# Performance work log

Hardware: AMD Instinct MI355X
Metric: run time of the kernel (lower is better)

## Reference

```python
import jax, jax.numpy as jnp
import numpy as np

NUM_EMBEDDINGS = 1024
EMBEDDING_DIM = 128
COMMITMENT_COST = 0.25


def setup_inputs() -> dict:
    key = jax.random.key(0)
    k1, k2 = jax.random.split(key)
    z = jax.random.normal(k1, (16, EMBEDDING_DIM, 64, 64), dtype=jnp.float32)
    # codebook initialized uniform(-1/K, 1/K) as in the torch module
    codebook = jax.random.uniform(
        k2, (NUM_EMBEDDINGS, EMBEDDING_DIM), dtype=jnp.float32,
        minval=-1.0 / NUM_EMBEDDINGS, maxval=1.0 / NUM_EMBEDDINGS)
    return {"z": z, "codebook": codebook}


def reference(z, codebook):
    B, C = z.shape[0], z.shape[1]
    K = codebook.shape[0]
    # (B, C, H, W) -> (B*H*W, C)
    z_flat = z.reshape(B, C, -1).transpose(0, 2, 1).reshape(-1, C)
    N = z_flat.shape[0]

    # squared L2 distances (same argmin as cdist p=2)
    d2 = (jnp.sum(z_flat * z_flat, axis=1, keepdims=True)
          - 2.0 * (z_flat @ codebook.T)
          + jnp.sum(codebook * codebook, axis=1))  # [N, K]
    indices = jnp.argmin(d2, axis=1)               # [N]

    quantized_flat = codebook[indices]             # [N, C] gather
    q_raw = quantized_flat.reshape(B, -1, C).transpose(0, 2, 1).reshape(z.shape)

    # training-mode losses (F.mse_loss = mean squared error)
    commitment_loss = jnp.mean((z - jax.lax.stop_gradient(q_raw)) ** 2)
    codebook_loss = jnp.mean((q_raw - jax.lax.stop_gradient(z)) ** 2)
    vq_loss = codebook_loss + COMMITMENT_COST * commitment_loss

    # straight-through estimator
    quantized = z + jax.lax.stop_gradient(q_raw - z)

    # perplexity over code usage (zero-count codes contribute 0 to entropy)
    counts = jax.ops.segment_sum(jnp.ones((N,), jnp.float32), indices,
                                 num_segments=K)
    probs = counts / jnp.float32(N)
    perplexity = jnp.exp(-jnp.sum(probs * jnp.log(probs + 1e-10)))

    return quantized, indices, vq_loss, perplexity
```

## Files before the change

### kernel.cpp

```cpp
#include <hip/hip_runtime.h>
#include <math.h>

namespace {
constexpr int CDIM   = 128;
constexpr int KCODES = 1024;
constexpr int HWSZ   = 4096;
constexpr int BATCH  = 16;
constexpr int NPOS   = BATCH * HWSZ;
constexpr int P      = 256;
constexpr int NWAVES = 8;
constexpr int KPW    = KCODES / NWAVES;
constexpr int THREADS = 512;
constexpr size_t QELEMS   = (size_t)BATCH * CDIM * HWSZ;
constexpr size_t IDX_OFF  = QELEMS;
constexpr size_t LOSS_OFF = IDX_OFF + (size_t)NPOS;
constexpr size_t PERP_OFF = LOSS_OFF + 1;
constexpr int WS_C2   = 0;
constexpr int WS_HIST = 1024;
constexpr int WS_LOSS = 2048;
constexpr float INV_TOTAL = 1.0f / (float)QELEMS;
constexpr float INV_NPOS  = 1.0f / (float)NPOS;
}

__device__ __forceinline__ float np_sumsq_128(const float* v) {
    float r[8];
    #pragma unroll
    for (int j = 0; j < 8; ++j) r[j] = __fmul_rn(v[j], v[j]);
    #pragma unroll
    for (int i = 8; i < 128; i += 8) {
        #pragma unroll
        for (int j = 0; j < 8; ++j)
            r[j] = __fadd_rn(r[j], __fmul_rn(v[i + j], v[i + j]));
    }
    const float s01 = __fadd_rn(r[0], r[1]);
    const float s23 = __fadd_rn(r[2], r[3]);
    const float s45 = __fadd_rn(r[4], r[5]);
    const float s67 = __fadd_rn(r[6], r[7]);
    return __fadd_rn(__fadd_rn(s01, s23), __fadd_rn(s45, s67));
}

__global__ __launch_bounds__(256) void vq_prep(const float* __restrict__ cb,
                                               float* __restrict__ ws) {
    const int k = blockIdx.x * 256 + threadIdx.x;
    const float* row = cb + (size_t)k * CDIM;
    float rr[CDIM];
    #pragma unroll
    for (int c = 0; c < CDIM; ++c) rr[c] = row[c];
    ws[WS_C2 + k] = np_sumsq_128(rr);
    ((unsigned int*)ws)[WS_HIST + k] = 0u;
    if (k == 0) ws[WS_LOSS] = 0.0f;
}

__global__ __launch_bounds__(512, 1) void vq_main(const float* __restrict__ z,
                                                  const float* __restrict__ cb,
                                                  float* __restrict__ ws,
                                                  float* __restrict__ out) {
    __shared__ __align__(16) float zt[CDIM][P];
    __shared__ float z2s[P];
    __shared__ float bdls[NWAVES][P];
    __shared__ int   bkls[NWAVES][P];
    __shared__ int   wkls[P];
    __shared__ float red[THREADS];

    const int tid   = threadIdx.x;
    const int nbase = blockIdx.x * P;
    const int b     = nbase >> 12;
    const int hw0   = nbase & (HWSZ - 1);
    const float* zb = z + (size_t)b * CDIM * HWSZ + hw0;

    #pragma unroll
    for (int i = 0; i < (CDIM * P / 4) / THREADS; ++i) {
        const int linear = i * THREADS + tid;
        const int c  = linear >> 6;
        const int p4 = (linear & 63) * 4;
        *(float4*)&zt[c][p4] = *(const float4*)(zb + (size_t)c * HWSZ + p4);
    }
    __syncthreads();

    if (tid < P) {
        const int p = tid;
        float r[8];
        #pragma unroll
        for (int j = 0; j < 8; ++j) {
            const float x = zt[j][p];
            r[j] = __fmul_rn(x, x);
        }
        #pragma unroll
        for (int i = 8; i < CDIM; i += 8) {
            #pragma unroll
            for (int j = 0; j < 8; ++j) {
                const float x = zt[i + j][p];
                r[j] = __fadd_rn(r[j], __fmul_rn(x, x));
            }
        }
        const float s01 = __fadd_rn(r[0], r[1]);
        const float s23 = __fadd_rn(r[2], r[3]);
        const float s45 = __fadd_rn(r[4], r[5]);
        const float s67 = __fadd_rn(r[6], r[7]);
        z2s[p] = __fadd_rn(__fadd_rn(s01, s23), __fadd_rn(s45, s67));
    }
    __syncthreads();

    const int lane = tid & 63;
    const int p0   = lane * 4;
    const int wid  = __builtin_amdgcn_readfirstlane(tid >> 6);
    const int kw   = wid * KPW;
    const float* c2g = ws + WS_C2;

    float z2r[4];
    #pragma unroll
    for (int i = 0; i < 4; ++i) z2r[i] = z2s[p0 + i];

    float bestd[4] = {INFINITY, INFINITY, INFINITY, INFINITY};
    int   bestk[4] = {0, 0, 0, 0};

    for (int oct = 0; oct < KPW / 8; ++oct) {
        const int kb = kw + oct * 8;
        const float* coct = cb + (size_t)kb * CDIM;

        float a[4][8];
        #pragma unroll
        for (int i = 0; i < 4; ++i)
            #pragma unroll
            for (int j = 0; j < 8; ++j) a[i][j] = 0.0f;

        #pragma unroll 2
        for (int c4 = 0; c4 < CDIM / 4; ++c4) {
            const int c = c4 * 4;
            const float4 zv0 = *(const float4*)&zt[c + 0][p0];
            const float4 zv1 = *(const float4*)&zt[c + 1][p0];
            const float4 zv2 = *(const float4*)&zt[c + 2][p0];
            const float4 zv3 = *(const float4*)&zt[c + 3][p0];
            float4 cv[8];
            #pragma unroll
            for (int j = 0; j < 8; ++j)
                cv[j] = *(const float4*)(coct + (size_t)j * CDIM + c);
            #pragma unroll
            for (int j = 0; j < 8; ++j) {
                a[0][j] = fmaf(zv0.x, cv[j].x, a[0][j]);
                a[0][j] = fmaf(zv1.x, cv[j].y, a[0][j]);
                a[0][j] = fmaf(zv2.x, cv[j].z, a[0][j]);
                a[0][j] = fmaf(zv3.x, cv[j].w, a[0][j]);
                a[1][j] = fmaf(zv0.y, cv[j].x, a[1][j]);
                a[1][j] = fmaf(zv1.y, cv[j].y, a[1][j]);
                a[1][j] = fmaf(zv2.y, cv[j].z, a[1][j]);
                a[1][j] = fmaf(zv3.y, cv[j].w, a[1][j]);
                a[2][j] = fmaf(zv0.z, cv[j].x, a[2][j]);
                a[2][j] = fmaf(zv1.z, cv[j].y, a[2][j]);
                a[2][j] = fmaf(zv2.z, cv[j].z, a[2][j]);
                a[2][j] = fmaf(zv3.z, cv[j].w, a[2][j]);
                a[3][j] = fmaf(zv0.w, cv[j].x, a[3][j]);
                a[3][j] = fmaf(zv1.w, cv[j].y, a[3][j]);
                a[3][j] = fmaf(zv2.w, cv[j].z, a[3][j]);
                a[3][j] = fmaf(zv3.w, cv[j].w, a[3][j]);
            }
        }

        #pragma unroll
        for (int j = 0; j < 8; ++j) {
            const float c2 = c2g[kb + j];
            #pragma unroll
            for (int i = 0; i < 4; ++i) {
                const float d = __fadd_rn(fmaf(-2.0f, a[i][j], z2r[i]), c2);
                if (d < bestd[i]) { bestd[i] = d; bestk[i] = kb + j; }
            }
        }
    }

    #pragma unroll
    for (int i = 0; i < 4; ++i) {
        bdls[wid][p0 + i] = bestd[i];
        bkls[wid][p0 + i] = bestk[i];
    }
    __syncthreads();

    unsigned int* ghist = (unsigned int*)ws + WS_HIST;
    if (tid < P) {
        const int p = tid;
        float bd = bdls[0][p];
        int   bk = bkls[0][p];
        #pragma unroll
        for (int g = 1; g < NWAVES; ++g) {
            const float d = bdls[g][p];
            const int   k = bkls[g][p];
            if (d < bd || (d == bd && k < bk)) { bd = d; bk = k; }
        }
        wkls[p] = bk;
        out[IDX_OFF + (size_t)(nbase + p)] = (float)bk;
        atomicAdd(&ghist[bk], 1u);
        red[tid] = bd;
    } else {
        red[tid] = 0.0f;
    }
    __syncthreads();
    for (int s = THREADS / 2; s > 0; s >>= 1) {
        if (tid < s) red[tid] += red[tid + s];
        __syncthreads();
    }
    if (tid == 0) atomicAdd(&ws[WS_LOSS], red[0]);

    float* ob = out + (size_t)b * CDIM * HWSZ + hw0;
    #pragma unroll
    for (int i = 0; i < (CDIM * P) / THREADS; ++i) {
        const int linear = i * THREADS + tid;
        const int c = linear >> 8;
        const int p = linear & 255;
        ob[(size_t)c * HWSZ + p] = cb[(size_t)wkls[p] * CDIM + c];
    }
}

__global__ __launch_bounds__(1024) void vq_final(const float* __restrict__ ws,
                                                 float* __restrict__ out) {
    __shared__ float red[1024];
    const int t = threadIdx.x;
    const unsigned int* hist = (const unsigned int*)ws + WS_HIST;
    const float p = (float)hist[t] * INV_NPOS;
    red[t] = p * logf(p + 1e-10f);
    __syncthreads();
    for (int s = 512; s > 0; s >>= 1) {
        if (t < s) red[t] += red[t + s];
        __syncthreads();
    }
    if (t == 0) {
        out[LOSS_OFF] = 1.25f * (ws[WS_LOSS] * INV_TOTAL);
        out[PERP_OFF] = expf(-red[0]);
    }
}

extern "C" void kernel_launch(void* const* d_in, const int* in_sizes, int n_in,
                              void* d_out, int out_size, void* d_ws, size_t ws_size,
                              hipStream_t stream) {
    const float* z  = (const float*)d_in[0];
    const float* cb = (const float*)d_in[1];
    float* out = (float*)d_out;
    float* ws  = (float*)d_ws;

    vq_prep <<<KCODES / 256, 256, 0, stream>>>(cb, ws);
    vq_main <<<NPOS / P,     THREADS, 0, stream>>>(z, cb, ws, out);
    vq_final<<<1,           1024, 0, stream>>>(ws, out);
}
```

Before: 302.6 us.

## Double waves per block to split codebook across sixteen waves

Raises the main kernel from 512 to 1024 threads per block, so sixteen waves each scan 64 codes instead of eight waves scanning 128. This aims to add latency hiding for the global codebook loads and FMA chains per CU. To fit the larger per-wave argmin staging into shared memory, the best-index arrays become 16-bit and the loss reduction buffer shrinks to P entries. Launch bounds of 1024 halve the register budget per thread, which may cause spills given the 32 accumulators plus the float4 codebook registers.

```diff
diff --git a/kernel.cpp b/kernel.cpp
--- a/kernel.cpp
+++ b/kernel.cpp
@@ -8,9 +8,10 @@
 constexpr int BATCH  = 16;
 constexpr int NPOS   = BATCH * HWSZ;
 constexpr int P      = 256;
-constexpr int NWAVES = 8;
+constexpr int NWAVES = 16;
 constexpr int KPW    = KCODES / NWAVES;
-constexpr int THREADS = 512;
+constexpr int KT     = 8;
+constexpr int THREADS = 1024;
 constexpr size_t QELEMS   = (size_t)BATCH * CDIM * HWSZ;
 constexpr size_t IDX_OFF  = QELEMS;
 constexpr size_t LOSS_OFF = IDX_OFF + (size_t)NPOS;
@@ -51,16 +52,16 @@
     if (k == 0) ws[WS_LOSS] = 0.0f;
 }
 
-__global__ __launch_bounds__(512, 1) void vq_main(const float* __restrict__ z,
-                                                  const float* __restrict__ cb,
-                                                  float* __restrict__ ws,
-                                                  float* __restrict__ out) {
+__global__ __launch_bounds__(1024, 1) void vq_main(const float* __restrict__ z,
+                                                   const float* __restrict__ cb,
+                                                   float* __restrict__ ws,
+                                                   float* __restrict__ out) {
     __shared__ __align__(16) float zt[CDIM][P];
     __shared__ float z2s[P];
     __shared__ float bdls[NWAVES][P];
-    __shared__ int   bkls[NWAVES][P];
-    __shared__ int   wkls[P];
-    __shared__ float red[THREADS];
+    __shared__ unsigned short bkls[NWAVES][P];
+    __shared__ unsigned short wkls[P];
+    __shared__ float red[P];
 
     const int tid   = threadIdx.x;
     const int nbase = blockIdx.x * P;
@@ -114,15 +115,15 @@
     float bestd[4] = {INFINITY, INFINITY, INFINITY, INFINITY};
     int   bestk[4] = {0, 0, 0, 0};
 
-    for (int oct = 0; oct < KPW / 8; ++oct) {
-        const int kb = kw + oct * 8;
-        const float* coct = cb + (size_t)kb * CDIM;
-
-        float a[4][8];
+    for (int ht = 0; ht < KPW / KT; ++ht) {
+        const int kb = kw + ht * KT;
+        const float* ctile = cb + (size_t)kb * CDIM;
+
+        float a[4][KT];
         #pragma unroll
         for (int i = 0; i < 4; ++i)
             #pragma unroll
-            for (int j = 0; j < 8; ++j) a[i][j] = 0.0f;
+            for (int j = 0; j < KT; ++j) a[i][j] = 0.0f;
 
         #pragma unroll 2
         for (int c4 = 0; c4 < CDIM / 4; ++c4) {
@@ -131,12 +132,12 @@
             const float4 zv1 = *(const float4*)&zt[c + 1][p0];
             const float4 zv2 = *(const float4*)&zt[c + 2][p0];
             const float4 zv3 = *(const float4*)&zt[c + 3][p0];
-            float4 cv[8];
-            #pragma unroll
-            for (int j = 0; j < 8; ++j)
-                cv[j] = *(const float4*)(coct + (size_t)j * CDIM + c);
-            #pragma unroll
-            for (int j = 0; j < 8; ++j) {
+            float4 cv[KT];
+            #pragma unroll
+            for (int j = 0; j < KT; ++j)
+                cv[j] = *(const float4*)(ctile + (size_t)j * CDIM + c);
+            #pragma unroll
+            for (int j = 0; j < KT; ++j) {
                 a[0][j] = fmaf(zv0.x, cv[j].x, a[0][j]);
                 a[0][j] = fmaf(zv1.x, cv[j].y, a[0][j]);
                 a[0][j] = fmaf(zv2.x, cv[j].z, a[0][j]);
@@ -157,7 +158,7 @@
         }
 
         #pragma unroll
-        for (int j = 0; j < 8; ++j) {
+        for (int j = 0; j < KT; ++j) {
             const float c2 = c2g[kb + j];
             #pragma unroll
             for (int i = 0; i < 4; ++i) {
@@ -170,7 +171,7 @@
     #pragma unroll
     for (int i = 0; i < 4; ++i) {
         bdls[wid][p0 + i] = bestd[i];
-        bkls[wid][p0 + i] = bestk[i];
+        bkls[wid][p0 + i] = (unsigned short)bestk[i];
     }
     __syncthreads();
 
@@ -185,15 +186,13 @@
             const int   k = bkls[g][p];
             if (d < bd || (d == bd && k < bk)) { bd = d; bk = k; }
         }
-        wkls[p] = bk;
+        wkls[p] = (unsigned short)bk;
         out[IDX_OFF + (size_t)(nbase + p)] = (float)bk;
         atomicAdd(&ghist[bk], 1u);
-        red[tid] = bd;
-    } else {
-        red[tid] = 0.0f;
-    }
-    __syncthreads();
-    for (int s = THREADS / 2; s > 0; s >>= 1) {
+        red[p] = bd;
+    }
+    __syncthreads();
+    for (int s = P / 2; s > 0; s >>= 1) {
         if (tid < s) red[tid] += red[tid + s];
         __syncthreads();
     }
```

After: 282.9 us. 1.07x faster.
